# Kernel tuning notes

Measured on AMD Instinct MI355X. Metric: run time of the kernel, lower is better.

## Reference

```python
import jax, jax.numpy as jnp
import numpy as np

B, S1, S2 = 1024, 25, 10          # batch, hop-1 fanout, hop-2 fanout
N, D, H, C = 100000, 256, 128, 64  # n_node, in_dim, per-branch out_dim, n_class


def setup_inputs() -> dict:
    key = jax.random.key(0)
    ks = jax.random.split(key, 10)
    rn = lambda k, shape: jax.random.normal(k, shape, dtype=jnp.float32) * 0.05
    return {
        "ids0": jax.random.randint(ks[0], (B,), 0, N),
        "ids1": jax.random.randint(ks[1], (B * S1,), 0, N),
        "ids2": jax.random.randint(ks[2], (B * S1 * S2,), 0, N),
        "features": jax.random.normal(ks[3], (N, D), dtype=jnp.float32),
        # aggregator layer 1 (in D, out 2H after concat)
        "Wx1": rn(ks[4], (D, H)), "bx1": jnp.zeros((H,), jnp.float32),
        "Wn1": rn(ks[5], (D, H)), "bn1": jnp.zeros((H,), jnp.float32),
        # aggregator layer 2 (in 2H, out 2H)
        "Wx2": rn(ks[6], (2 * H, H)), "bx2": jnp.zeros((H,), jnp.float32),
        "Wn2": rn(ks[7], (2 * H, H)), "bn2": jnp.zeros((H,), jnp.float32),
        # final linear head
        "Wfc": rn(ks[8], (2 * H, C)), "bfc": jnp.zeros((C,), jnp.float32),
    }


def _mean_agg(x, neibs, Wx, bx, Wn, bn, act):
    # neibs: [x_rows * fanout, d] -> mean over fanout, then concat of two linears
    n = neibs.reshape(x.shape[0], -1, neibs.shape[-1]).mean(axis=1)
    out = jnp.concatenate([x @ Wx + bx, n @ Wn + bn], axis=-1)
    return act(out)


def reference(ids0, ids1, ids2, features,
              Wx1, bx1, Wn1, bn1, Wx2, bx2, Wn2, bn2, Wfc, bfc):
    # hop-wise feature gathers (identity prep)
    h0 = features[ids0]   # [B, D]
    h1 = features[ids1]   # [B*S1, D]
    h2 = features[ids2]   # [B*S1*S2, D]
    # layer 1 aggregation (relu), applied to consecutive hop pairs
    g0 = _mean_agg(h0, h1, Wx1, bx1, Wn1, bn1, jax.nn.relu)   # [B, 2H]
    g1 = _mean_agg(h1, h2, Wx1, bx1, Wn1, bn1, jax.nn.relu)   # [B*S1, 2H]
    # layer 2 aggregation (identity activation on last layer)
    f0 = _mean_agg(g0, g1, Wx2, bx2, Wn2, bn2, lambda v: v)   # [B, 2H]
    return f0 @ Wfc + bfc  # [B, C]
```

## Files before the change

kernel.cpp:

```cpp
#include <hip/hip_runtime.h>

#define DD 256
#define HH 128
#define CC 64
#define BB 1024
#define SS1 25
#define SS2 10
#define NN 100000

typedef __attribute__((ext_vector_type(8))) short bf16x8;
typedef __attribute__((ext_vector_type(4))) float f32x4;

__device__ inline unsigned short f2b(float x) {
    union { float f; unsigned u; } v; v.f = x;
    unsigned r = (v.u + 0x7fffu + ((v.u >> 16) & 1u)) >> 16;
    return (unsigned short)r;
}
__device__ inline float b2f(unsigned u16) {
    union { unsigned u; float f; } v; v.u = u16 << 16;
    return v.f;
}

__global__ __launch_bounds__(256)
void prep_w(const float* __restrict__ Wx, const float* __restrict__ Wn,
            unsigned short* __restrict__ Wsw) {
    const int t    = blockIdx.x * 256 + threadIdx.x;
    const int lane = t & 63;
    const int frag = t >> 6;
    const int kc = frag >> 4, nt = frag & 15;
    const int quad = lane >> 4, lr = lane & 15;
    unsigned short v[8];
#pragma unroll
    for (int j = 0; j < 8; ++j) {
        int k = kc * 32 + quad * 8 + j;
        int n = nt * 16 + lr;
        float w = (n < HH) ? Wx[k * HH + n] : Wn[k * HH + (n - HH)];
        v[j] = f2b(w);
    }
    ((uint4*)Wsw)[t] = *(uint4*)v;
}

#define PQ_BLOCKS 512
#define PQ_TILES  (NN / 32)
#define AS 264

#define PQ_ISSUE(VREG, TIDX)                                                  \
    {                                                                         \
        const float* fn_ = feat + (long)(TIDX) * 32 * DD + sc * 8;            \
        _Pragma("unroll")                                                     \
        for (int i_ = 0; i_ < 4; ++i_) {                                      \
            const float4* s_ = (const float4*)(fn_ + (long)(i_ * 8 + srow) * DD); \
            VREG[2 * i_]     = s_[0];                                         \
            VREG[2 * i_ + 1] = s_[1];                                         \
        }                                                                     \
    }

#define PQ_STEP(VREG)                                                         \
    {                                                                         \
              \
        _Pragma("unroll")                                                     \
        for (int i_ = 0; i_ < 4; ++i_) {                                      \
            int row_ = i_ * 8 + srow;                                         \
            float4 a_ = VREG[2 * i_], b_ = VREG[2 * i_ + 1];                  \
            unsigned short w8_[8] = { f2b(a_.x), f2b(a_.y), f2b(a_.z), f2b(a_.w), \
                                      f2b(b_.x), f2b(b_.y), f2b(b_.z), f2b(b_.w) }; \
            *(uint4*)&sAO[0][row_ * AS + sc * 8] = *(uint4*)w8_;              \
        }                                                                     \
                                \
        {                                                                     \
            long t2_ = tile + 2L * PQ_BLOCKS;                                 \
            if (t2_ < PQ_TILES) PQ_ISSUE(VREG, t2_);                          \
        }                                                                     \
                       \
        asm volatile("s_waitcnt lgkmcnt(0)" ::: "memory");                    \
        __builtin_amdgcn_s_barrier();                                         \
                                          \
        f32x4 acc[2][4] = {};                                                 \
        _Pragma("unroll")                                                     \
        for (int kc = 0; kc < 8; ++kc) {                                      \
            bf16x8 a0 = *(const bf16x8*)&sAO[0][(lr)      * AS + kc * 32 + quad * 8]; \
            bf16x8 a1 = *(const bf16x8*)&sAO[0][(16 + lr) * AS + kc * 32 + quad * 8]; \
            _Pragma("unroll")                                                 \
            for (int j = 0; j < 4; ++j) {                                     \
                acc[0][j] = __builtin_amdgcn_mfma_f32_16x16x32_bf16(a0, B[kc][j], acc[0][j], 0, 0, 0); \
                acc[1][j] = __builtin_amdgcn_mfma_f32_16x16x32_bf16(a1, B[kc][j], acc[1][j], 0, 0, 0); \
            }                                                                 \
        }                                                                     \
                  \
        _Pragma("unroll")                                                     \
        for (int rt = 0; rt < 2; ++rt)                                        \
            _Pragma("unroll")                                                 \
            for (int j = 0; j < 4; ++j) {                                     \
                int col_ = (w * 4 + j) * 16 + lr;                             \
                _Pragma("unroll")                                             \
                for (int r = 0; r < 4; ++r)                                   \
                    sAO[1][(rt * 16 + quad * 4 + r) * AS + col_] = f2b(acc[rt][j][r]); \
            }                                                                 \
                  \
        asm volatile("s_waitcnt lgkmcnt(0)" ::: "memory");                    \
        __builtin_amdgcn_s_barrier();                                         \
                                           \
        _Pragma("unroll")                                                     \
        for (int i_ = 0; i_ < 4; ++i_) {                                      \
            int id_  = i_ * 256 + t;                                          \
            int row_ = id_ >> 5, ch_ = id_ & 31;                              \
            uint4 d_ = *(uint4*)&sAO[1][row_ * AS + ch_ * 8];                 \
            *(uint4*)&PQb[((long)tile * 32 + row_) * DD + ch_ * 8] = d_;      \
        }                                                                     \
    }

__global__ __launch_bounds__(256, 2)
void pq_gemm(const float* __restrict__ feat,
             const unsigned short* __restrict__ Wsw,
             unsigned short* __restrict__ PQb) {
    __shared__ unsigned short sAO[2][32 * AS];
    const int t    = threadIdx.x;
    const int w    = t >> 6, lane = t & 63;
    const int quad = lane >> 4, lr = lane & 15;

    bf16x8 B[8][4];
#pragma unroll
    for (int kc = 0; kc < 8; ++kc)
#pragma unroll
        for (int j = 0; j < 4; ++j)
            B[kc][j] = *(const bf16x8*)&Wsw[((kc * 16 + (w * 4 + j)) * 64 + lane) * 8];

    const int srow = t >> 5, sc = t & 31;

    float4 va[8], vb[8];
    long tile = blockIdx.x;
    PQ_ISSUE(va, tile);
    if (tile + PQ_BLOCKS < PQ_TILES) PQ_ISSUE(vb, tile + PQ_BLOCKS);

    while (true) {
        PQ_STEP(va);
        tile += PQ_BLOCKS; if (tile >= PQ_TILES) break;
        PQ_STEP(vb);
        tile += PQ_BLOCKS; if (tile >= PQ_TILES) break;
    }
}

__global__ __launch_bounds__(512)
void megatail(const unsigned short* __restrict__ PQb,
              const int* __restrict__ ids0, const int* __restrict__ ids1,
              const int* __restrict__ ids2,
              const float* __restrict__ bx1, const float* __restrict__ bn1,
              const float* __restrict__ Wx2, const float* __restrict__ bx2,
              const float* __restrict__ Wn2, const float* __restrict__ bn2,
              const float* __restrict__ Wfc, const float* __restrict__ bfc,
              float* __restrict__ out) {
    __shared__ float sred[8][3 * HH];
    __shared__ float g0L[DD];
    __shared__ float gmL[DD];
    __shared__ float FP[2][DD];
    __shared__ float FL[DD];
    __shared__ float sp[8][CC];
    const int i    = blockIdx.x;
    const int t    = threadIdx.x;
    const int wv   = t >> 6, lane = t & 63;
    const int l16  = lane & 15;
    const int slot = wv * 4 + (lane >> 4);
    const int c0   = l16 * 8;

    float xs[8], ns[8], g0n[8];
#pragma unroll
    for (int k = 0; k < 8; ++k) { xs[k] = 0.f; ns[k] = 0.f; g0n[k] = 0.f; }

    if (slot < SS1) {
        const int row = i * SS1 + slot;
        const long xr = (long)ids1[row];
        uint4 xv  = *(const uint4*)&PQb[xr * DD + c0];
        uint4 nv0 = *(const uint4*)&PQb[xr * DD + HH + c0];
        int myid = ids2[row * SS2 + (l16 % SS2)];
        float pa[8];
#pragma unroll
        for (int k = 0; k < 8; ++k) pa[k] = 0.f;
#pragma unroll
        for (int j = 0; j < SS2; ++j) {
            long nr = (long)__shfl(myid, (lane & 48) + j);
            uint4 nv = *(const uint4*)&PQb[nr * DD + HH + c0];
            pa[0] += b2f(nv.x & 0xffff); pa[1] += b2f(nv.x >> 16);
            pa[2] += b2f(nv.y & 0xffff); pa[3] += b2f(nv.y >> 16);
            pa[4] += b2f(nv.z & 0xffff); pa[5] += b2f(nv.z >> 16);
            pa[6] += b2f(nv.w & 0xffff); pa[7] += b2f(nv.w >> 16);
        }
        const float4 bxa = *(const float4*)&bx1[c0];
        const float4 bxb = *(const float4*)&bx1[c0 + 4];
        const float4 bna = *(const float4*)&bn1[c0];
        const float4 bnb = *(const float4*)&bn1[c0 + 4];
        constexpr float inv2 = 1.f / SS2;
        xs[0] = fmaxf(b2f(xv.x & 0xffff) + bxa.x, 0.f);
        xs[1] = fmaxf(b2f(xv.x >> 16)    + bxa.y, 0.f);
        xs[2] = fmaxf(b2f(xv.y & 0xffff) + bxa.z, 0.f);
        xs[3] = fmaxf(b2f(xv.y >> 16)    + bxa.w, 0.f);
        xs[4] = fmaxf(b2f(xv.z & 0xffff) + bxb.x, 0.f);
        xs[5] = fmaxf(b2f(xv.z >> 16)    + bxb.y, 0.f);
        xs[6] = fmaxf(b2f(xv.w & 0xffff) + bxb.z, 0.f);
        xs[7] = fmaxf(b2f(xv.w >> 16)    + bxb.w, 0.f);
        ns[0] = fmaxf(pa[0] * inv2 + bna.x, 0.f);
        ns[1] = fmaxf(pa[1] * inv2 + bna.y, 0.f);
        ns[2] = fmaxf(pa[2] * inv2 + bna.z, 0.f);
        ns[3] = fmaxf(pa[3] * inv2 + bna.w, 0.f);
        ns[4] = fmaxf(pa[4] * inv2 + bnb.x, 0.f);
        ns[5] = fmaxf(pa[5] * inv2 + bnb.y, 0.f);
        ns[6] = fmaxf(pa[6] * inv2 + bnb.z, 0.f);
        ns[7] = fmaxf(pa[7] * inv2 + bnb.w, 0.f);
        g0n[0] = b2f(nv0.x & 0xffff); g0n[1] = b2f(nv0.x >> 16);
        g0n[2] = b2f(nv0.y & 0xffff); g0n[3] = b2f(nv0.y >> 16);
        g0n[4] = b2f(nv0.z & 0xffff); g0n[5] = b2f(nv0.z >> 16);
        g0n[6] = b2f(nv0.w & 0xffff); g0n[7] = b2f(nv0.w >> 16);
    }

#pragma unroll
    for (int k = 0; k < 8; ++k) {
        xs[k]  += __shfl_xor(xs[k], 16);  xs[k]  += __shfl_xor(xs[k], 32);
        ns[k]  += __shfl_xor(ns[k], 16);  ns[k]  += __shfl_xor(ns[k], 32);
        g0n[k] += __shfl_xor(g0n[k], 16); g0n[k] += __shfl_xor(g0n[k], 32);
    }
    if (lane < 16) {
        *(float4*)&sred[wv][c0]              = make_float4(xs[0], xs[1], xs[2], xs[3]);
        *(float4*)&sred[wv][c0 + 4]          = make_float4(xs[4], xs[5], xs[6], xs[7]);
        *(float4*)&sred[wv][HH + c0]         = make_float4(ns[0], ns[1], ns[2], ns[3]);
        *(float4*)&sred[wv][HH + c0 + 4]     = make_float4(ns[4], ns[5], ns[6], ns[7]);
        *(float4*)&sred[wv][2 * HH + c0]     = make_float4(g0n[0], g0n[1], g0n[2], g0n[3]);
        *(float4*)&sred[wv][2 * HH + c0 + 4] = make_float4(g0n[4], g0n[5], g0n[6], g0n[7]);
    }
    __syncthreads();

    if (t < 384) {
        float r = 0.f;
#pragma unroll
        for (int k = 0; k < 8; ++k) r += sred[k][t];
        if (t < 256) {
            gmL[t] = r * (1.f / SS1);
        } else {
            const int c = t - 256;
            g0L[HH + c] = fmaxf(r * (1.f / SS1) + bn1[c], 0.f);
        }
    } else {
        const int c = t - 384;
        unsigned short u = PQb[(long)ids0[i] * DD + c];
        g0L[c] = fmaxf(b2f(u) + bx1[c], 0.f);
    }
    __syncthreads();

    {
        const int c = t & 255, h = t >> 8;
        const bool xhalf = (c < HH);
        const float* __restrict__ W    = xhalf ? Wx2 : Wn2;
        const float* __restrict__ srcL = xhalf ? g0L : gmL;
        const int cc = c & (HH - 1);
        float fa = 0.f;
#pragma unroll 8
        for (int k = h * 128; k < h * 128 + 128; ++k) fa += srcL[k] * W[k * HH + cc];
        FP[h][c] = fa;
    }
    __syncthreads();
    if (t < 256)
        FL[t] = FP[0][t] + FP[1][t] + ((t < HH) ? bx2[t] : bn2[t - HH]);
    __syncthreads();

    {
        const int col = t & (CC - 1), q = t >> 6;
        float p = 0.f;
#pragma unroll 8
        for (int k = q * 32; k < q * 32 + 32; ++k) p += FL[k] * Wfc[k * CC + col];
        sp[q][col] = p;
    }
    __syncthreads();
    if (t < CC) {
        float r = bfc[t];
#pragma unroll
        for (int q = 0; q < 8; ++q) r += sp[q][t];
        out[(long)i * CC + t] = r;
    }
}

extern "C" void kernel_launch(void* const* d_in, const int* in_sizes, int n_in,
                              void* d_out, int out_size, void* d_ws, size_t ws_size,
                              hipStream_t stream) {
    const int*   ids0 = (const int*)d_in[0];
    const int*   ids1 = (const int*)d_in[1];
    const int*   ids2 = (const int*)d_in[2];
    const float* feat = (const float*)d_in[3];
    const float* Wx1  = (const float*)d_in[4];
    const float* bx1  = (const float*)d_in[5];
    const float* Wn1  = (const float*)d_in[6];
    const float* bn1  = (const float*)d_in[7];
    const float* Wx2  = (const float*)d_in[8];
    const float* bx2  = (const float*)d_in[9];
    const float* Wn2  = (const float*)d_in[10];
    const float* bn2  = (const float*)d_in[11];
    const float* Wfc  = (const float*)d_in[12];
    const float* bfc  = (const float*)d_in[13];
    float* out = (float*)d_out;

    unsigned short* PQb = (unsigned short*)d_ws;
    unsigned short* Wsw = PQb + (long)NN * DD;

    prep_w<<<32, 256, 0, stream>>>(Wx1, Wn1, Wsw);
    pq_gemm<<<PQ_BLOCKS, 256, 0, stream>>>(feat, Wsw, PQb);
    megatail<<<BB, 512, 0, stream>>>(PQb, ids0, ids1, ids2, bx1, bn1,
                                     Wx2, bx2, Wn2, bn2, Wfc, bfc, out);
}
```

Baseline: 219.0 us.

## Split PQ GEMM output columns across block pairs to raise occupancy

Each 32-row tile of the feature projection is split into two tasks, one per 128-column half (Wx1 or Wn1). Each block keeps half the weight fragments in registers, and the grid grows from 512 to 1536 blocks with 3 blocks per CU. The double-buffered register prefetch is reduced to a single buffer to free registers. The aim is more waves in flight to hide the feature-load latency. The cost is that every feature tile is read and converted to bf16 twice, once per column half, which roughly doubles the dominant read traffic unless the second read hits cache.

```diff
diff --git a/kernel.cpp b/kernel.cpp
--- a/kernel.cpp
+++ b/kernel.cpp
@@ -40,103 +40,102 @@
     ((uint4*)Wsw)[t] = *(uint4*)v;
 }
 
-#define PQ_BLOCKS 512
+#define PQ_GRID   1536
 #define PQ_TILES  (NN / 32)
+#define PQ_TASKS  (PQ_TILES * 2)
 #define AS 264
-
-#define PQ_ISSUE(VREG, TIDX)                                                  \
-    {                                                                         \
-        const float* fn_ = feat + (long)(TIDX) * 32 * DD + sc * 8;            \
-        _Pragma("unroll")                                                     \
-        for (int i_ = 0; i_ < 4; ++i_) {                                      \
-            const float4* s_ = (const float4*)(fn_ + (long)(i_ * 8 + srow) * DD); \
-            VREG[2 * i_]     = s_[0];                                         \
-            VREG[2 * i_ + 1] = s_[1];                                         \
-        }                                                                     \
-    }
-
-#define PQ_STEP(VREG)                                                         \
-    {                                                                         \
-              \
-        _Pragma("unroll")                                                     \
-        for (int i_ = 0; i_ < 4; ++i_) {                                      \
-            int row_ = i_ * 8 + srow;                                         \
-            float4 a_ = VREG[2 * i_], b_ = VREG[2 * i_ + 1];                  \
-            unsigned short w8_[8] = { f2b(a_.x), f2b(a_.y), f2b(a_.z), f2b(a_.w), \
-                                      f2b(b_.x), f2b(b_.y), f2b(b_.z), f2b(b_.w) }; \
-            *(uint4*)&sAO[0][row_ * AS + sc * 8] = *(uint4*)w8_;              \
-        }                                                                     \
-                                \
-        {                                                                     \
-            long t2_ = tile + 2L * PQ_BLOCKS;                                 \
-            if (t2_ < PQ_TILES) PQ_ISSUE(VREG, t2_);                          \
-        }                                                                     \
-                       \
-        asm volatile("s_waitcnt lgkmcnt(0)" ::: "memory");                    \
-        __builtin_amdgcn_s_barrier();                                         \
-                                          \
-        f32x4 acc[2][4] = {};                                                 \
-        _Pragma("unroll")                                                     \
-        for (int kc = 0; kc < 8; ++kc) {                                      \
-            bf16x8 a0 = *(const bf16x8*)&sAO[0][(lr)      * AS + kc * 32 + quad * 8]; \
-            bf16x8 a1 = *(const bf16x8*)&sAO[0][(16 + lr) * AS + kc * 32 + quad * 8]; \
-            _Pragma("unroll")                                                 \
-            for (int j = 0; j < 4; ++j) {                                     \
-                acc[0][j] = __builtin_amdgcn_mfma_f32_16x16x32_bf16(a0, B[kc][j], acc[0][j], 0, 0, 0); \
-                acc[1][j] = __builtin_amdgcn_mfma_f32_16x16x32_bf16(a1, B[kc][j], acc[1][j], 0, 0, 0); \
-            }                                                                 \
-        }                                                                     \
-                  \
-        _Pragma("unroll")                                                     \
-        for (int rt = 0; rt < 2; ++rt)                                        \
-            _Pragma("unroll")                                                 \
-            for (int j = 0; j < 4; ++j) {                                     \
-                int col_ = (w * 4 + j) * 16 + lr;                             \
-                _Pragma("unroll")                                             \
-                for (int r = 0; r < 4; ++r)                                   \
-                    sAO[1][(rt * 16 + quad * 4 + r) * AS + col_] = f2b(acc[rt][j][r]); \
-            }                                                                 \
-                  \
-        asm volatile("s_waitcnt lgkmcnt(0)" ::: "memory");                    \
-        __builtin_amdgcn_s_barrier();                                         \
-                                           \
-        _Pragma("unroll")                                                     \
-        for (int i_ = 0; i_ < 4; ++i_) {                                      \
-            int id_  = i_ * 256 + t;                                          \
-            int row_ = id_ >> 5, ch_ = id_ & 31;                              \
-            uint4 d_ = *(uint4*)&sAO[1][row_ * AS + ch_ * 8];                 \
-            *(uint4*)&PQb[((long)tile * 32 + row_) * DD + ch_ * 8] = d_;      \
-        }                                                                     \
-    }
-
-__global__ __launch_bounds__(256, 2)
+#define OS 132
+
+__global__ __launch_bounds__(256, 3)
 void pq_gemm(const float* __restrict__ feat,
              const unsigned short* __restrict__ Wsw,
              unsigned short* __restrict__ PQb) {
-    __shared__ unsigned short sAO[2][32 * AS];
+    __shared__ unsigned short sA[32 * AS];
+    __shared__ unsigned short sO[32 * OS];
     const int t    = threadIdx.x;
     const int w    = t >> 6, lane = t & 63;
     const int quad = lane >> 4, lr = lane & 15;
-
-    bf16x8 B[8][4];
+    const int by   = blockIdx.x & 1;
+
+    bf16x8 B[8][2];
 #pragma unroll
     for (int kc = 0; kc < 8; ++kc)
 #pragma unroll
-        for (int j = 0; j < 4; ++j)
-            B[kc][j] = *(const bf16x8*)&Wsw[((kc * 16 + (w * 4 + j)) * 64 + lane) * 8];
+        for (int j = 0; j < 2; ++j) {
+            int nt = by * 8 + w * 2 + j;
+            B[kc][j] = *(const bf16x8*)&Wsw[((kc * 16 + nt) * 64 + lane) * 8];
+        }
 
     const int srow = t >> 5, sc = t & 31;
 
-    float4 va[8], vb[8];
-    long tile = blockIdx.x;
-    PQ_ISSUE(va, tile);
-    if (tile + PQ_BLOCKS < PQ_TILES) PQ_ISSUE(vb, tile + PQ_BLOCKS);
-
+    float4 v[8];
+    long task = blockIdx.x;
+    {
+        const float* fb = feat + (task >> 1) * 32 * DD + sc * 8;
+#pragma unroll
+        for (int i = 0; i < 4; ++i) {
+            const float4* src = (const float4*)(fb + (long)(i * 8 + srow) * DD);
+            v[2 * i]     = src[0];
+            v[2 * i + 1] = src[1];
+        }
+    }
+
+#pragma unroll 1
     while (true) {
-        PQ_STEP(va);
-        tile += PQ_BLOCKS; if (tile >= PQ_TILES) break;
-        PQ_STEP(vb);
-        tile += PQ_BLOCKS; if (tile >= PQ_TILES) break;
+        const long tile = task >> 1;
+#pragma unroll
+        for (int i = 0; i < 4; ++i) {
+            int row = i * 8 + srow;
+            float4 a = v[2 * i], b = v[2 * i + 1];
+            unsigned short w8[8] = { f2b(a.x), f2b(a.y), f2b(a.z), f2b(a.w),
+                                     f2b(b.x), f2b(b.y), f2b(b.z), f2b(b.w) };
+            *(uint4*)&sA[row * AS + sc * 8] = *(uint4*)w8;
+        }
+        long tn = task + PQ_GRID;
+        if (tn < PQ_TASKS) {
+            const float* fn = feat + (tn >> 1) * 32 * DD + sc * 8;
+#pragma unroll
+            for (int i = 0; i < 4; ++i) {
+                const float4* src = (const float4*)(fn + (long)(i * 8 + srow) * DD);
+                v[2 * i]     = src[0];
+                v[2 * i + 1] = src[1];
+            }
+        }
+        asm volatile("s_waitcnt lgkmcnt(0)" ::: "memory");
+        __builtin_amdgcn_s_barrier();
+
+        f32x4 acc[2][2] = {};
+#pragma unroll
+        for (int kc = 0; kc < 8; ++kc) {
+            bf16x8 a0 = *(const bf16x8*)&sA[(lr)      * AS + kc * 32 + quad * 8];
+            bf16x8 a1 = *(const bf16x8*)&sA[(16 + lr) * AS + kc * 32 + quad * 8];
+#pragma unroll
+            for (int j = 0; j < 2; ++j) {
+                acc[0][j] = __builtin_amdgcn_mfma_f32_16x16x32_bf16(a0, B[kc][j], acc[0][j], 0, 0, 0);
+                acc[1][j] = __builtin_amdgcn_mfma_f32_16x16x32_bf16(a1, B[kc][j], acc[1][j], 0, 0, 0);
+            }
+        }
+#pragma unroll
+        for (int rt = 0; rt < 2; ++rt)
+#pragma unroll
+            for (int j = 0; j < 2; ++j) {
+                int col = (w * 2 + j) * 16 + lr;
+#pragma unroll
+                for (int r = 0; r < 4; ++r)
+                    sO[(rt * 16 + quad * 4 + r) * OS + col] = f2b(acc[rt][j][r]);
+            }
+        asm volatile("s_waitcnt lgkmcnt(0)" ::: "memory");
+        __builtin_amdgcn_s_barrier();
+
+#pragma unroll
+        for (int i = 0; i < 2; ++i) {
+            int id  = i * 256 + t;
+            int row = id >> 4, ch = id & 15;
+            uint4 d = *(uint4*)&sO[row * OS + ch * 8];
+            *(uint4*)&PQb[(tile * 32 + row) * DD + by * HH + ch * 8] = d;
+        }
+        task = tn;
+        if (task >= PQ_TASKS) break;
     }
 }
 
@@ -299,7 +298,7 @@
     unsigned short* Wsw = PQb + (long)NN * DD;
 
     prep_w<<<32, 256, 0, stream>>>(Wx1, Wn1, Wsw);
-    pq_gemm<<<PQ_BLOCKS, 256, 0, stream>>>(feat, Wsw, PQb);
+    pq_gemm<<<PQ_GRID, 256, 0, stream>>>(feat, Wsw, PQb);
     megatail<<<BB, 512, 0, stream>>>(PQb, ids0, ids1, ids2, bx1, bn1,
                                      Wx2, bx2, Wn2, bn2, Wfc, bfc, out);
 }
```

New measurement: 221.7 us. About the same (+1.2%).
